# Performance work log

Hardware: AMD Instinct MI355X
Metric: run time of the kernel (lower is better)

The kernel has to match this reference:

```python
import jax, jax.numpy as jnp
import numpy as np

N = 50000        # nodes
E = 800000       # edges
D_IN = 128       # input feature dim
HID = 64         # hidden_dim
HEADS = 4
OUT = 2          # output_dim (fraud / not-fraud)
BN_EPS = 1e-5
NEG_SLOPE = 0.2  # PyG GATv2Conv default


def setup_inputs() -> dict:
    key = jax.random.key(0)
    ks = jax.random.split(key, 16)
    g = lambda k, shape, s=0.05: (jax.random.normal(k, shape, jnp.float32) * s)
    HC = HEADS * HID  # 256
    return {
        "x": jax.random.normal(ks[0], (N, D_IN), jnp.float32),
        "edge_index": jax.random.randint(ks[1], (2, E), 0, N),
        # input projection
        "W_in": g(ks[2], (D_IN, HID)), "b_in": jnp.zeros((HID,), jnp.float32),
        # GATv2 layer 0: HID -> HID, 4 heads (concat -> 256)
        "Wl0": g(ks[3], (HID, HC)), "Wr0": g(ks[4], (HID, HC)),
        "att0": g(ks[5], (HEADS, HID)), "bias0": jnp.zeros((HC,), jnp.float32),
        # GATv2 layer 1: 256 -> HID, 4 heads (concat -> 256)
        "Wl1": g(ks[6], (HC, HC)), "Wr1": g(ks[7], (HC, HC)),
        "att1": g(ks[8], (HEADS, HID)), "bias1": jnp.zeros((HC,), jnp.float32),
        # GATv2 layer 2: 256 -> OUT, 1 head
        "Wl2": g(ks[9], (HC, OUT)), "Wr2": g(ks[10], (HC, OUT)),
        "att2": g(ks[11], (1, OUT)), "bias2": jnp.zeros((OUT,), jnp.float32),
        # BatchNorm (eval mode: running stats) for the first num_layers-1 = 2 layers
        "bn_gamma": jnp.ones((2, HC), jnp.float32),
        "bn_beta": jnp.zeros((2, HC), jnp.float32),
        "bn_mean": jnp.zeros((2, HC), jnp.float32),
        "bn_var": jnp.ones((2, HC), jnp.float32),
    }


def _gatv2(h, src, dst, Wl, Wr, att, bias):
    """PyG GATv2Conv (concat=True, negative_slope=0.2). src->dst messages."""
    n = h.shape[0]
    heads, c = att.shape
    xl = (h @ Wl).reshape(n, heads, c)   # source transform
    xr = (h @ Wr).reshape(n, heads, c)   # target transform
    e = jax.nn.leaky_relu(xl[src] + xr[dst], NEG_SLOPE)       # [E, H, C]
    logits = jnp.einsum('ehc,hc->eh', e, att)                 # [E, H]
    # segment softmax over incoming edges of each destination node
    m = jax.ops.segment_max(logits, dst, num_segments=n)      # [N, H]
    ex = jnp.exp(logits - m[dst])
    denom = jax.ops.segment_sum(ex, dst, num_segments=n)
    alpha = ex / denom[dst]                                   # [E, H]
    out = jax.ops.segment_sum(xl[src] * alpha[..., None], dst, num_segments=n)
    return out.reshape(n, heads * c) + bias


def _bn_eval(h, gamma, beta, mean, var):
    return gamma * (h - mean) * jax.lax.rsqrt(var + BN_EPS) + beta


def reference(x, edge_index, W_in, b_in, Wl0, Wr0, att0, bias0,
              Wl1, Wr1, att1, bias1, Wl2, Wr2, att2, bias2,
              bn_gamma, bn_beta, bn_mean, bn_var):
    n = x.shape[0]
    loop = jnp.arange(n)
    src = jnp.concatenate([edge_index[0], loop])  # PyG add_self_loops=True
    dst = jnp.concatenate([edge_index[1], loop])

    h = jax.nn.relu(x @ W_in + b_in)              # dropout is identity in eval

    # layer 0 (no residual: 64 != 256)
    h = _gatv2(h, src, dst, Wl0, Wr0, att0, bias0)
    h = jax.nn.relu(_bn_eval(h, bn_gamma[0], bn_beta[0], bn_mean[0], bn_var[0]))

    # layer 1 (residual: 256 == 256)
    h_prev = h
    h = _gatv2(h, src, dst, Wl1, Wr1, att1, bias1)
    h = jax.nn.relu(_bn_eval(h, bn_gamma[1], bn_beta[1], bn_mean[1], bn_var[1]))
    h = h + h_prev

    # output layer, 1 head
    h = _gatv2(h, src, dst, Wl2, Wr2, att2, bias2)
    return jax.nn.log_softmax(h, axis=1)
```

## Files before the change

kernel.cpp:

```cpp
#include <hip/hip_runtime.h>
#include <hip/hip_bf16.h>
#include <math.h>


using h16     = _Float16;
using half2v  = __attribute__((ext_vector_type(2))) h16;
using half4v  = __attribute__((ext_vector_type(4))) h16;
using half8   = __attribute__((ext_vector_type(8))) h16;
using floatx2 = __attribute__((ext_vector_type(2))) float;
using floatx4 = __attribute__((ext_vector_type(4))) float;

__device__ __forceinline__ float lrelu(float x) { return x > 0.f ? x : 0.2f * x; }

__device__ __forceinline__ half2v shfl_xor_h2(half2v v, int mask) {
    float f = __builtin_bit_cast(float, v);
    f = __shfl_xor(f, mask, 64);
    return __builtin_bit_cast(half2v, f);
}

__device__ __forceinline__ half4v cvt_fp8x4(unsigned v) {
    floatx2 lo = __builtin_amdgcn_cvt_pk_f32_fp8((int)v, false);
    floatx2 hi = __builtin_amdgcn_cvt_pk_f32_fp8((int)v, true);
    half4v r = { (h16)lo.x, (h16)lo.y, (h16)hi.x, (h16)hi.y };
    return r;
}

__global__ void hist_dst(const int* __restrict__ ei, int E, int* __restrict__ deg) {
    int e = blockIdx.x * blockDim.x + threadIdx.x;
    if (e < E) atomicAdd(&deg[ei[E + e]], 1);
}

__global__ __launch_bounds__(256) void scan_blk(const int* __restrict__ deg,
                                                int* __restrict__ rowstart,
                                                int* __restrict__ bsum, int N) {
    int t = blockIdx.x * 256 + threadIdx.x;
    int lane = threadIdx.x & 63, wid = threadIdx.x >> 6;
    int v = (t < N) ? ((deg[t] + 4) & ~3) : 0;
    int x = v;
#pragma unroll
    for (int off = 1; off < 64; off <<= 1) {
        int y = __shfl_up(x, off, 64);
        if (lane >= off) x += y;
    }
    __shared__ int wsum[4];
    if (lane == 63) wsum[wid] = x;
    __syncthreads();
    int add = 0;
#pragma unroll
    for (int w = 0; w < 4; ++w) if (w < wid) add += wsum[w];
    int incl = x + add;
    if (t < N) rowstart[t] = incl - v;
    if (threadIdx.x == 255) bsum[blockIdx.x] = incl;
}

__global__ __launch_bounds__(256) void scan_off(int* __restrict__ bsum, int NB) {
    int t = threadIdx.x;
    int lane = t & 63, wid = t >> 6;
    int v = (t < NB) ? bsum[t] : 0;
    int x = v;
#pragma unroll
    for (int off = 1; off < 64; off <<= 1) {
        int y = __shfl_up(x, off, 64);
        if (lane >= off) x += y;
    }
    __shared__ int wsum[4];
    if (lane == 63) wsum[wid] = x;
    __syncthreads();
    int add = 0;
#pragma unroll
    for (int w = 0; w < 4; ++w) if (w < wid) add += wsum[w];
    if (t < NB) bsum[t] = x + add - v;
}

__global__ void add_off(const int* __restrict__ bsum, const int* __restrict__ deg,
                        int* __restrict__ rowstart, int* __restrict__ cursor,
                        int* __restrict__ csr_src, int N) {
    int t = blockIdx.x * 256 + threadIdx.x;
    if (t >= N) return;
    int r = rowstart[t] + bsum[blockIdx.x];
    rowstart[t] = r;
    cursor[t] = r;
    int dg = deg[t];
    int npad = (dg + 4) & ~3;
    for (int k = dg; k < npad; ++k) csr_src[r + k] = t;
}

__global__ void scatter_src(const int* __restrict__ ei, int E,
                            int* __restrict__ cursor, int* __restrict__ csr_src) {
    int e = blockIdx.x * blockDim.x + threadIdx.x;
    if (e >= E) return;
    int d = ei[E + e];
    int pos = atomicAdd(&cursor[d], 1);
    csr_src[pos] = ei[e];
}

__device__ __forceinline__ void pack_one(const float* __restrict__ W,
                                         h16* __restrict__ Wp,
                                         int t, int K, int NC) {
    int j = t & 7;
    int l = (t >> 3) & 63;
    int rest = t >> 9;
    int NT = NC >> 4;
    int nt = rest % NT;
    int kc = rest / NT;
    int row = kc * 32 + (l >> 4) * 8 + j;
    int col = nt * 16 + (l & 15);
    Wp[t] = (h16)W[(size_t)row * NC + col];
}

__global__ void pack_all(const float* __restrict__ W_in,
                         const float* __restrict__ Wl0, const float* __restrict__ Wr0,
                         const float* __restrict__ Wl1, const float* __restrict__ Wr1,
                         h16* __restrict__ P_in,
                         h16* __restrict__ P_l0, h16* __restrict__ P_r0,
                         h16* __restrict__ P_l1, h16* __restrict__ P_r1,
                         const float4* __restrict__ x, half4v* __restrict__ xh, int n4,
                         int* __restrict__ deg, int N) {
    int t = blockIdx.x * blockDim.x + threadIdx.x;
    if (t < 8192)        pack_one(W_in, P_in, t, 128, 64);
    else if (t < 24576)  pack_one(Wl0, P_l0, t - 8192, 64, 256);
    else if (t < 40960)  pack_one(Wr0, P_r0, t - 24576, 64, 256);
    else if (t < 106496) pack_one(Wl1, P_l1, t - 40960, 256, 256);
    else if (t < 172032) pack_one(Wr1, P_r1, t - 106496, 256, 256);
    else if (t < 172032 + n4) {
        int u = t - 172032;
        float4 v = x[u];
        half4v o = { (h16)v.x, (h16)v.y, (h16)v.z, (h16)v.w };
        xh[u] = o;
    } else {
        int u = t - 172032 - n4;
        if (u < N) deg[u] = 0;
    }
}

template<int KC, int NT, bool RELU, bool DUAL, bool OUT8>
__global__ __launch_bounds__(256) void gemm_lds(
        const h16* __restrict__ Xh,
        const h16* __restrict__ Wp0, const h16* __restrict__ Wp1,
        const float* __restrict__ bias,
        void* __restrict__ out0v, void* __restrict__ out1v, int M) {
    constexpr int K = KC * 32;
    constexpr int ldo = NT * 16;
    constexpr int CHUNK8 = NT * 64;
    constexpr int PER_THR = CHUNK8 / 256;
    __shared__ half8 wbuf[2][CHUNK8];

    const h16* Wp = (DUAL && blockIdx.y) ? Wp1 : Wp0;
    void* outv = (DUAL && blockIdx.y) ? out1v : out0v;
    const half8* WG = (const half8*)Wp;

    const int tid = threadIdx.x;
    const int wid = tid >> 6, lane = tid & 63;
    const int quad = lane >> 4, li = lane & 15;
    const int r0 = blockIdx.x * 64 + wid * 16;
    int arow = r0 + li; if (arow >= M) arow = M - 1;
    const half8* A8 = (const half8*)Xh + (size_t)arow * (K / 8) + quad;

    floatx4 acc[NT];
#pragma unroll
    for (int t = 0; t < NT; ++t) acc[t] = (floatx4){0.f, 0.f, 0.f, 0.f};

    half8 st[PER_THR];
#pragma unroll
    for (int i = 0; i < PER_THR; ++i) st[i] = WG[i * 256 + tid];
#pragma unroll
    for (int i = 0; i < PER_THR; ++i) wbuf[0][i * 256 + tid] = st[i];
    __syncthreads();

#pragma unroll
    for (int kc = 0; kc < KC; ++kc) {
        int cur = kc & 1;
        if (kc + 1 < KC) {
#pragma unroll
            for (int i = 0; i < PER_THR; ++i)
                st[i] = WG[(size_t)(kc + 1) * CHUNK8 + i * 256 + tid];
        }
        half8 a = A8[kc * 4];
#pragma unroll
        for (int nt = 0; nt < NT; ++nt) {
            half8 b = wbuf[cur][nt * 64 + lane];
            acc[nt] = __builtin_amdgcn_mfma_f32_16x16x32_f16(a, b, acc[nt], 0, 0, 0);
        }
        if (kc + 1 < KC) {
#pragma unroll
            for (int i = 0; i < PER_THR; ++i) wbuf[cur ^ 1][i * 256 + tid] = st[i];
        }
        __syncthreads();
    }

#pragma unroll
    for (int nt = 0; nt < NT; ++nt) {
#pragma unroll
        for (int reg = 0; reg < 4; ++reg) {
            int rr = r0 + quad * 4 + reg;
            if (rr >= M) continue;
            float v = acc[nt][reg];
            if (RELU) v = fmaxf(v + bias[nt * 16 + li], 0.f);
            if (OUT8) {
                int pk = __builtin_amdgcn_cvt_pk_fp8_f32(v, v, 0, false);
                ((unsigned char*)outv)[(size_t)rr * ldo + nt * 16 + li] = (unsigned char)pk;
            } else {
                ((h16*)outv)[(size_t)rr * ldo + nt * 16 + li] = (h16)v;
            }
        }
    }
}

__global__ void attn4_bn(int N, const unsigned char* __restrict__ XL8,
                         const unsigned char* __restrict__ XR8,
                         const float* __restrict__ att,
                         const int* __restrict__ rowstart, const int* __restrict__ deg,
                         const int* __restrict__ csr_src,
                         const float* __restrict__ gamma, const float* __restrict__ beta,
                         const float* __restrict__ mean, const float* __restrict__ var,
                         const float* __restrict__ bias, const float* __restrict__ resid,
                         float* __restrict__ out, h16* __restrict__ outb) {
    int d = blockIdx.x * (blockDim.x >> 6) + (threadIdx.x >> 6);
    int lane = threadIdx.x & 63;
    if (d >= N) return;
    const unsigned* XL32 = (const unsigned*)XL8;
    unsigned bw = ((const unsigned*)(XR8 + (size_t)d * 256))[lane];
    half4v bv = cvt_fp8x4(bw);
    float4 wf = ((const float4*)att)[lane];
    half2v b0 = bv.xy, b1 = bv.zw;
    half2v w0 = { (h16)wf.x, (h16)wf.y };
    half2v w1 = { (h16)wf.z, (h16)wf.w };
    const h16 k02 = (h16)0.2f;

    auto edge_part = [&](half4v xv) -> h16 {
        half2v e0 = xv.xy + b0, e1 = xv.zw + b1;
        half2v l0 = __builtin_elementwise_max(e0, e0 * k02);
        half2v l1 = __builtin_elementwise_max(e1, e1 * k02);
        half2v qd = l0 * w0 + l1 * w1;
        return qd.x + qd.y;
    };

    int start = rowstart[d];
    int nreal = deg[d] + 1;
    int npad  = (deg[d] + 4) & ~3;
    float l = 0.f;
    half2v acc0 = { (h16)0.f, (h16)0.f };
    half2v acc1 = { (h16)0.f, (h16)0.f };

    int4 iv = *(const int4*)(csr_src + start);
    for (int i = 0; i < npad; i += 8) {
        int4 ia = iv;
        int4 ib = ia;
        if (i + 4 < npad) ib = *(const int4*)(csr_src + start + i + 4);
        if (i + 8 < npad) iv = *(const int4*)(csr_src + start + i + 8);
        unsigned va0 = XL32[(size_t)ia.x * 64 + lane];
        unsigned va1 = XL32[(size_t)ia.y * 64 + lane];
        unsigned va2 = XL32[(size_t)ia.z * 64 + lane];
        unsigned va3 = XL32[(size_t)ia.w * 64 + lane];
        unsigned vb0 = XL32[(size_t)ib.x * 64 + lane];
        unsigned vb1 = XL32[(size_t)ib.y * 64 + lane];
        unsigned vb2 = XL32[(size_t)ib.z * 64 + lane];
        unsigned vb3 = XL32[(size_t)ib.w * 64 + lane];
        half4v x0 = cvt_fp8x4(va0);
        half4v x1 = cvt_fp8x4(va1);
        half4v x2 = cvt_fp8x4(va2);
        half4v x3 = cvt_fp8x4(va3);
        half4v x4 = cvt_fp8x4(vb0);
        half4v x5 = cvt_fp8x4(vb1);
        half4v x6 = cvt_fp8x4(vb2);
        half4v x7 = cvt_fp8x4(vb3);
        half2v p01 = { edge_part(x0), edge_part(x1) };
        half2v p23 = { edge_part(x2), edge_part(x3) };
        half2v p45 = { edge_part(x4), edge_part(x5) };
        half2v p67 = { edge_part(x6), edge_part(x7) };
#pragma unroll
        for (int s = 1; s < 16; s <<= 1) {
            p01 += shfl_xor_h2(p01, s);
            p23 += shfl_xor_h2(p23, s);
            p45 += shfl_xor_h2(p45, s);
            p67 += shfl_xor_h2(p67, s);
        }
        int rem = nreal - i;
        float e0 = __expf((float)p01.x);
        float e1 = (rem > 1) ? __expf((float)p01.y) : 0.f;
        float e2 = (rem > 2) ? __expf((float)p23.x) : 0.f;
        float e3 = (rem > 3) ? __expf((float)p23.y) : 0.f;
        float e4 = (rem > 4) ? __expf((float)p45.x) : 0.f;
        float e5 = (rem > 5) ? __expf((float)p45.y) : 0.f;
        float e6 = (rem > 6) ? __expf((float)p67.x) : 0.f;
        float e7 = (rem > 7) ? __expf((float)p67.y) : 0.f;
        l += ((e0 + e1) + (e2 + e3)) + ((e4 + e5) + (e6 + e7));
        h16 h0 = (h16)e0, h1 = (h16)e1, h2 = (h16)e2, h3 = (h16)e3;
        h16 h4 = (h16)e4, h5 = (h16)e5, h6 = (h16)e6, h7 = (h16)e7;
        half2v eb0 = { h0, h0 }, eb1 = { h1, h1 }, eb2 = { h2, h2 }, eb3 = { h3, h3 };
        half2v eb4 = { h4, h4 }, eb5 = { h5, h5 }, eb6 = { h6, h6 }, eb7 = { h7, h7 };
        acc0 += eb0 * x0.xy; acc1 += eb0 * x0.zw;
        acc0 += eb1 * x1.xy; acc1 += eb1 * x1.zw;
        acc0 += eb2 * x2.xy; acc1 += eb2 * x2.zw;
        acc0 += eb3 * x3.xy; acc1 += eb3 * x3.zw;
        acc0 += eb4 * x4.xy; acc1 += eb4 * x4.zw;
        acc0 += eb5 * x5.xy; acc1 += eb5 * x5.zw;
        acc0 += eb6 * x6.xy; acc1 += eb6 * x6.zw;
        acc0 += eb7 * x7.xy; acc1 += eb7 * x7.zw;
    }
    float4 acc = { (float)acc0.x, (float)acc0.y, (float)acc1.x, (float)acc1.y };
    float inv = 1.f / l;
    float4 g  = ((const float4*)gamma)[lane];
    float4 be = ((const float4*)beta)[lane];
    float4 mu = ((const float4*)mean)[lane];
    float4 va = ((const float4*)var)[lane];
    float4 bi = ((const float4*)bias)[lane];
    float4 sc4, sh4;
    sc4.x = g.x * rsqrtf(va.x + 1e-5f); sh4.x = (bi.x - mu.x) * sc4.x + be.x;
    sc4.y = g.y * rsqrtf(va.y + 1e-5f); sh4.y = (bi.y - mu.y) * sc4.y + be.y;
    sc4.z = g.z * rsqrtf(va.z + 1e-5f); sh4.z = (bi.z - mu.z) * sc4.z + be.z;
    sc4.w = g.w * rsqrtf(va.w + 1e-5f); sh4.w = (bi.w - mu.w) * sc4.w + be.w;
    float4 o;
    o.x = fmaxf(acc.x * inv * sc4.x + sh4.x, 0.f);
    o.y = fmaxf(acc.y * inv * sc4.y + sh4.y, 0.f);
    o.z = fmaxf(acc.z * inv * sc4.z + sh4.z, 0.f);
    o.w = fmaxf(acc.w * inv * sc4.w + sh4.w, 0.f);
    if (resid) {
        float4 rv = *(const float4*)(resid + (size_t)d * 256 + lane * 4);
        o.x += rv.x; o.y += rv.y; o.z += rv.z; o.w += rv.w;
    }
    if (out) *(float4*)(out + (size_t)d * 256 + lane * 4) = o;
    if (outb) {
        half4v ob = { (h16)o.x, (h16)o.y, (h16)o.z, (h16)o.w };
        *(half4v*)(outb + (size_t)d * 256 + lane * 4) = ob;
    }
}

__global__ void gemm2_wave(const h16* __restrict__ X, const float* __restrict__ Wl,
                           const float* __restrict__ Wr, float* __restrict__ xl2,
                           float* __restrict__ xr2, int N) {
    int t = blockIdx.x * blockDim.x + threadIdx.x;
    int n = t >> 4;
    int sl = t & 15;
    if (n >= N) return;
    const half4v* Xr = (const half4v*)(X + (size_t)n * 256);
    const float4* Wl4 = (const float4*)Wl;
    const float4* Wr4 = (const float4*)Wr;
    float l0 = 0.f, l1 = 0.f, r0 = 0.f, r1 = 0.f;
#pragma unroll
    for (int j = 0; j < 4; ++j) {
        int idx = sl + j * 16;
        half4v xh = Xr[idx];
        float4 xv = { (float)xh.x, (float)xh.y, (float)xh.z, (float)xh.w };
        float4 wa = Wl4[idx * 2];
        float4 wb = Wl4[idx * 2 + 1];
        l0 += xv.x * wa.x + xv.y * wa.z + xv.z * wb.x + xv.w * wb.z;
        l1 += xv.x * wa.y + xv.y * wa.w + xv.z * wb.y + xv.w * wb.w;
        wa = Wr4[idx * 2]; wb = Wr4[idx * 2 + 1];
        r0 += xv.x * wa.x + xv.y * wa.z + xv.z * wb.x + xv.w * wb.z;
        r1 += xv.x * wa.y + xv.y * wa.w + xv.z * wb.y + xv.w * wb.w;
    }
#pragma unroll
    for (int off = 1; off < 16; off <<= 1) {
        l0 += __shfl_xor(l0, off, 64);
        l1 += __shfl_xor(l1, off, 64);
        r0 += __shfl_xor(r0, off, 64);
        r1 += __shfl_xor(r1, off, 64);
    }
    if (sl == 0) {
        xl2[n * 2] = l0; xl2[n * 2 + 1] = l1;
        xr2[n * 2] = r0; xr2[n * 2 + 1] = r1;
    }
}

__global__ void attn1_16(int N, const float* __restrict__ xl2, const float* __restrict__ xr2,
                         const float* __restrict__ att, const float* __restrict__ bias,
                         const int* __restrict__ rowstart, const int* __restrict__ deg,
                         const int* __restrict__ csr_src, float* __restrict__ out) {
    int t = blockIdx.x * blockDim.x + threadIdx.x;
    int d = t >> 4, sl = t & 15;
    if (d >= N) return;
    float a0 = att[0], a1 = att[1];
    float2 xr = ((const float2*)xr2)[d];
    float b0 = xr.x, b1 = xr.y;
    int st = rowstart[d];
    int nreal = deg[d] + 1;
    int npad  = (deg[d] + 4) & ~3;
    float l = 0.f, ac0 = 0.f, ac1 = 0.f;
    for (int i = sl; i < npad; i += 16) {
        int s = csr_src[st + i];
        float2 xv = ((const float2*)xl2)[s];
        float q = lrelu(xv.x + b0) * a0 + lrelu(xv.y + b1) * a1;
        float e = (i < nreal) ? __expf(q) : 0.f;
        l += e; ac0 += e * xv.x; ac1 += e * xv.y;
    }
#pragma unroll
    for (int off = 1; off < 16; off <<= 1) {
        l   += __shfl_xor(l, off, 64);
        ac0 += __shfl_xor(ac0, off, 64);
        ac1 += __shfl_xor(ac1, off, 64);
    }
    if (sl == 0) {
        float inv = 1.f / l;
        float v0 = ac0 * inv + bias[0];
        float v1 = ac1 * inv + bias[1];
        float mx = fmaxf(v0, v1);
        float lse = mx + logf(__expf(v0 - mx) + __expf(v1 - mx));
        out[d * 2] = v0 - lse;
        out[d * 2 + 1] = v1 - lse;
    }
}

extern "C" void kernel_launch(void* const* d_in, const int* in_sizes, int n_in,
                              void* d_out, int out_size, void* d_ws, size_t ws_size,
                              hipStream_t stream) {
    const float* x        = (const float*)d_in[0];
    const int*   ei       = (const int*)  d_in[1];
    const float* W_in     = (const float*)d_in[2];
    const float* b_in     = (const float*)d_in[3];
    const float* Wl0      = (const float*)d_in[4];
    const float* Wr0      = (const float*)d_in[5];
    const float* att0     = (const float*)d_in[6];
    const float* bias0    = (const float*)d_in[7];
    const float* Wl1      = (const float*)d_in[8];
    const float* Wr1      = (const float*)d_in[9];
    const float* att1     = (const float*)d_in[10];
    const float* bias1    = (const float*)d_in[11];
    const float* Wl2      = (const float*)d_in[12];
    const float* Wr2      = (const float*)d_in[13];
    const float* att2     = (const float*)d_in[14];
    const float* bias2    = (const float*)d_in[15];
    const float* bn_gamma = (const float*)d_in[16];
    const float* bn_beta  = (const float*)d_in[17];
    const float* bn_mean  = (const float*)d_in[18];
    const float* bn_var   = (const float*)d_in[19];

    const int N  = in_sizes[0] / 128;
    const int E  = in_sizes[1] / 2;
    const int NB = (N + 255) / 256;

    float* ws = (float*)d_ws;
    size_t off = 0;
    float* C    = ws + off; off += (size_t)N * 256;
    float* XL2  = ws + off; off += (size_t)N * 2;
    float* XR2  = ws + off; off += (size_t)N * 2;
    unsigned char* A8 = (unsigned char*)(ws + off); off += (size_t)N * 64;
    unsigned char* B8 = (unsigned char*)(ws + off); off += (size_t)N * 64;
    h16* Ch   = (h16*)(ws + off); off += (size_t)N * 128;
    h16* Dh   = (h16*)(ws + off); off += (size_t)N * 128;
    h16* H0h  = (h16*)(ws + off); off += (size_t)N * 32;
    h16* xh   = (h16*)(ws + off); off += (size_t)N * 64;
    h16* Wp_in = (h16*)(ws + off); off += 4096;
    h16* Wp_l0 = (h16*)(ws + off); off += 8192;
    h16* Wp_r0 = (h16*)(ws + off); off += 8192;
    h16* Wp_l1 = (h16*)(ws + off); off += 32768;
    h16* Wp_r1 = (h16*)(ws + off); off += 32768;
    int* ip = (int*)(ws + off);
    int* deg      = ip;              ip += N;
    int* rowstart = ip;              ip += N;
    int* cursor   = ip;              ip += N;
    int* bsum     = ip;              ip += NB;
    int* csr_src  = ip;              ip += E + 4 * N + 64;

    const int PACK_T = 172032 + N * 32 + N;
    pack_all<<<(PACK_T + 255) / 256, 256, 0, stream>>>(
        W_in, Wl0, Wr0, Wl1, Wr1, Wp_in, Wp_l0, Wp_r0, Wp_l1, Wp_r1,
        (const float4*)x, (half4v*)xh, N * 32, deg, N);

    hist_dst<<<(E + 255) / 256, 256, 0, stream>>>(ei, E, deg);
    scan_blk<<<NB, 256, 0, stream>>>(deg, rowstart, bsum, N);
    scan_off<<<1, 256, 0, stream>>>(bsum, NB);
    add_off<<<NB, 256, 0, stream>>>(bsum, deg, rowstart, cursor, csr_src, N);
    scatter_src<<<(E + 255) / 256, 256, 0, stream>>>(ei, E, cursor, csr_src);

    const int GBM = (N + 63) / 64;

    gemm_lds<4, 4, true, false, false><<<GBM, 256, 0, stream>>>(
        xh, Wp_in, nullptr, b_in, H0h, nullptr, N);

    gemm_lds<2, 16, false, true, true><<<dim3(GBM, 2), 256, 0, stream>>>(
        H0h, Wp_l0, Wp_r0, nullptr, A8, B8, N);
    attn4_bn<<<(N + 3) / 4, 256, 0, stream>>>(N, A8, B8, att0, rowstart, deg, csr_src,
                                              bn_gamma, bn_beta, bn_mean, bn_var,
                                              bias0, nullptr, C, Ch);

    gemm_lds<8, 16, false, true, true><<<dim3(GBM, 2), 256, 0, stream>>>(
        Ch, Wp_l1, Wp_r1, nullptr, A8, B8, N);
    attn4_bn<<<(N + 3) / 4, 256, 0, stream>>>(N, A8, B8, att1, rowstart, deg, csr_src,
                                              bn_gamma + 256, bn_beta + 256, bn_mean + 256,
                                              bn_var + 256, bias1, C, nullptr, Dh);

    gemm2_wave<<<(N * 16 + 255) / 256, 256, 0, stream>>>(Dh, Wl2, Wr2, XL2, XR2, N);
    attn1_16<<<(N * 16 + 255) / 256, 256, 0, stream>>>(N, XL2, XR2, att2, bias2,
                                                       rowstart, deg, csr_src, (float*)d_out);
}
```

Measured before the change: 424.2 us.

## Store GAT projections in fp16 instead of fp8 and drop fp32 residual buffer

The dual projection GEMMs now write fp16 XL/XR instead of fp8, so the attention kernel loads 8 bytes per lane and skips the fp8-to-half conversion. The residual path now reads the fp16 layer-0 output instead of a separate fp32 copy, which removes that fp32 write and read. The gather loop processes 4 edges per iteration instead of 8. This doubles the gather traffic for neighbour features and lowers memory-level parallelism per iteration, in exchange for better accuracy and fewer conversion instructions.

```diff
diff --git a/kernel.cpp b/kernel.cpp
--- a/kernel.cpp
+++ b/kernel.cpp
@@ -16,13 +16,6 @@
     float f = __builtin_bit_cast(float, v);
     f = __shfl_xor(f, mask, 64);
     return __builtin_bit_cast(half2v, f);
-}
-
-__device__ __forceinline__ half4v cvt_fp8x4(unsigned v) {
-    floatx2 lo = __builtin_amdgcn_cvt_pk_f32_fp8((int)v, false);
-    floatx2 hi = __builtin_amdgcn_cvt_pk_f32_fp8((int)v, true);
-    half4v r = { (h16)lo.x, (h16)lo.y, (h16)hi.x, (h16)hi.y };
-    return r;
 }
 
 __global__ void hist_dst(const int* __restrict__ ei, int E, int* __restrict__ deg) {
@@ -133,12 +126,12 @@
     }
 }
 
-template<int KC, int NT, bool RELU, bool DUAL, bool OUT8>
+template<int KC, int NT, bool RELU, bool DUAL>
 __global__ __launch_bounds__(256) void gemm_lds(
         const h16* __restrict__ Xh,
         const h16* __restrict__ Wp0, const h16* __restrict__ Wp1,
         const float* __restrict__ bias,
-        void* __restrict__ out0v, void* __restrict__ out1v, int M) {
+        h16* __restrict__ out0, h16* __restrict__ out1, int M) {
     constexpr int K = KC * 32;
     constexpr int ldo = NT * 16;
     constexpr int CHUNK8 = NT * 64;
@@ -146,7 +139,7 @@
     __shared__ half8 wbuf[2][CHUNK8];
 
     const h16* Wp = (DUAL && blockIdx.y) ? Wp1 : Wp0;
-    void* outv = (DUAL && blockIdx.y) ? out1v : out0v;
+    h16* outp = (DUAL && blockIdx.y) ? out1 : out0;
     const half8* WG = (const half8*)Wp;
 
     const int tid = threadIdx.x;
@@ -196,31 +189,25 @@
             if (rr >= M) continue;
             float v = acc[nt][reg];
             if (RELU) v = fmaxf(v + bias[nt * 16 + li], 0.f);
-            if (OUT8) {
-                int pk = __builtin_amdgcn_cvt_pk_fp8_f32(v, v, 0, false);
-                ((unsigned char*)outv)[(size_t)rr * ldo + nt * 16 + li] = (unsigned char)pk;
-            } else {
-                ((h16*)outv)[(size_t)rr * ldo + nt * 16 + li] = (h16)v;
-            }
+            outp[(size_t)rr * ldo + nt * 16 + li] = (h16)v;
         }
     }
 }
 
-__global__ void attn4_bn(int N, const unsigned char* __restrict__ XL8,
-                         const unsigned char* __restrict__ XR8,
+__global__ void attn4_bn(int N, const h16* __restrict__ XL,
+                         const h16* __restrict__ XR,
                          const float* __restrict__ att,
                          const int* __restrict__ rowstart, const int* __restrict__ deg,
                          const int* __restrict__ csr_src,
                          const float* __restrict__ gamma, const float* __restrict__ beta,
                          const float* __restrict__ mean, const float* __restrict__ var,
-                         const float* __restrict__ bias, const float* __restrict__ resid,
-                         float* __restrict__ out, h16* __restrict__ outb) {
+                         const float* __restrict__ bias, const h16* __restrict__ resid,
+                         h16* __restrict__ outb) {
     int d = blockIdx.x * (blockDim.x >> 6) + (threadIdx.x >> 6);
     int lane = threadIdx.x & 63;
     if (d >= N) return;
-    const unsigned* XL32 = (const unsigned*)XL8;
-    unsigned bw = ((const unsigned*)(XR8 + (size_t)d * 256))[lane];
-    half4v bv = cvt_fp8x4(bw);
+    const uint2* XL64 = (const uint2*)XL;
+    half4v bv = *(const half4v*)(XR + (size_t)d * 256 + lane * 4);
     float4 wf = ((const float4*)att)[lane];
     half2v b0 = bv.xy, b1 = bv.zw;
     half2v w0 = { (h16)wf.x, (h16)wf.y };
@@ -243,60 +230,36 @@
     half2v acc1 = { (h16)0.f, (h16)0.f };
 
     int4 iv = *(const int4*)(csr_src + start);
-    for (int i = 0; i < npad; i += 8) {
-        int4 ia = iv;
-        int4 ib = ia;
-        if (i + 4 < npad) ib = *(const int4*)(csr_src + start + i + 4);
-        if (i + 8 < npad) iv = *(const int4*)(csr_src + start + i + 8);
-        unsigned va0 = XL32[(size_t)ia.x * 64 + lane];
-        unsigned va1 = XL32[(size_t)ia.y * 64 + lane];
-        unsigned va2 = XL32[(size_t)ia.z * 64 + lane];
-        unsigned va3 = XL32[(size_t)ia.w * 64 + lane];
-        unsigned vb0 = XL32[(size_t)ib.x * 64 + lane];
-        unsigned vb1 = XL32[(size_t)ib.y * 64 + lane];
-        unsigned vb2 = XL32[(size_t)ib.z * 64 + lane];
-        unsigned vb3 = XL32[(size_t)ib.w * 64 + lane];
-        half4v x0 = cvt_fp8x4(va0);
-        half4v x1 = cvt_fp8x4(va1);
-        half4v x2 = cvt_fp8x4(va2);
-        half4v x3 = cvt_fp8x4(va3);
-        half4v x4 = cvt_fp8x4(vb0);
-        half4v x5 = cvt_fp8x4(vb1);
-        half4v x6 = cvt_fp8x4(vb2);
-        half4v x7 = cvt_fp8x4(vb3);
+    for (int i = 0; i < npad; i += 4) {
+        int4 cur = iv;
+        if (i + 4 < npad) iv = *(const int4*)(csr_src + start + i + 4);
+        uint2 v0 = XL64[(size_t)cur.x * 64 + lane];
+        uint2 v1 = XL64[(size_t)cur.y * 64 + lane];
+        uint2 v2 = XL64[(size_t)cur.z * 64 + lane];
+        uint2 v3 = XL64[(size_t)cur.w * 64 + lane];
+        half4v x0 = __builtin_bit_cast(half4v, v0);
+        half4v x1 = __builtin_bit_cast(half4v, v1);
+        half4v x2 = __builtin_bit_cast(half4v, v2);
+        half4v x3 = __builtin_bit_cast(half4v, v3);
         half2v p01 = { edge_part(x0), edge_part(x1) };
         half2v p23 = { edge_part(x2), edge_part(x3) };
-        half2v p45 = { edge_part(x4), edge_part(x5) };
-        half2v p67 = { edge_part(x6), edge_part(x7) };
 #pragma unroll
         for (int s = 1; s < 16; s <<= 1) {
             p01 += shfl_xor_h2(p01, s);
             p23 += shfl_xor_h2(p23, s);
-            p45 += shfl_xor_h2(p45, s);
-            p67 += shfl_xor_h2(p67, s);
         }
         int rem = nreal - i;
         float e0 = __expf((float)p01.x);
         float e1 = (rem > 1) ? __expf((float)p01.y) : 0.f;
         float e2 = (rem > 2) ? __expf((float)p23.x) : 0.f;
         float e3 = (rem > 3) ? __expf((float)p23.y) : 0.f;
-        float e4 = (rem > 4) ? __expf((float)p45.x) : 0.f;
-        float e5 = (rem > 5) ? __expf((float)p45.y) : 0.f;
-        float e6 = (rem > 6) ? __expf((float)p67.x) : 0.f;
-        float e7 = (rem > 7) ? __expf((float)p67.y) : 0.f;
-        l += ((e0 + e1) + (e2 + e3)) + ((e4 + e5) + (e6 + e7));
+        l += (e0 + e1) + (e2 + e3);
         h16 h0 = (h16)e0, h1 = (h16)e1, h2 = (h16)e2, h3 = (h16)e3;
-        h16 h4 = (h16)e4, h5 = (h16)e5, h6 = (h16)e6, h7 = (h16)e7;
         half2v eb0 = { h0, h0 }, eb1 = { h1, h1 }, eb2 = { h2, h2 }, eb3 = { h3, h3 };
-        half2v eb4 = { h4, h4 }, eb5 = { h5, h5 }, eb6 = { h6, h6 }, eb7 = { h7, h7 };
         acc0 += eb0 * x0.xy; acc1 += eb0 * x0.zw;
         acc0 += eb1 * x1.xy; acc1 += eb1 * x1.zw;
         acc0 += eb2 * x2.xy; acc1 += eb2 * x2.zw;
         acc0 += eb3 * x3.xy; acc1 += eb3 * x3.zw;
-        acc0 += eb4 * x4.xy; acc1 += eb4 * x4.zw;
-        acc0 += eb5 * x5.xy; acc1 += eb5 * x5.zw;
-        acc0 += eb6 * x6.xy; acc1 += eb6 * x6.zw;
-        acc0 += eb7 * x7.xy; acc1 += eb7 * x7.zw;
     }
     float4 acc = { (float)acc0.x, (float)acc0.y, (float)acc1.x, (float)acc1.y };
     float inv = 1.f / l;
@@ -316,14 +279,12 @@
     o.z = fmaxf(acc.z * inv * sc4.z + sh4.z, 0.f);
     o.w = fmaxf(acc.w * inv * sc4.w + sh4.w, 0.f);
     if (resid) {
-        float4 rv = *(const float4*)(resid + (size_t)d * 256 + lane * 4);
-        o.x += rv.x; o.y += rv.y; o.z += rv.z; o.w += rv.w;
-    }
-    if (out) *(float4*)(out + (size_t)d * 256 + lane * 4) = o;
-    if (outb) {
-        half4v ob = { (h16)o.x, (h16)o.y, (h16)o.z, (h16)o.w };
-        *(half4v*)(outb + (size_t)d * 256 + lane * 4) = ob;
-    }
+        half4v rv = *(const half4v*)(resid + (size_t)d * 256 + lane * 4);
+        o.x += (float)rv.x; o.y += (float)rv.y;
+        o.z += (float)rv.z; o.w += (float)rv.w;
+    }
+    half4v ob = { (h16)o.x, (h16)o.y, (h16)o.z, (h16)o.w };
+    *(half4v*)(outb + (size_t)d * 256 + lane * 4) = ob;
 }
 
 __global__ void gemm2_wave(const h16* __restrict__ X, const float* __restrict__ Wl,
@@ -431,11 +392,10 @@
 
     float* ws = (float*)d_ws;
     size_t off = 0;
-    float* C    = ws + off; off += (size_t)N * 256;
     float* XL2  = ws + off; off += (size_t)N * 2;
     float* XR2  = ws + off; off += (size_t)N * 2;
-    unsigned char* A8 = (unsigned char*)(ws + off); off += (size_t)N * 64;
-    unsigned char* B8 = (unsigned char*)(ws + off); off += (size_t)N * 64;
+    h16* Ah   = (h16*)(ws + off); off += (size_t)N * 128;
+    h16* Bh   = (h16*)(ws + off); off += (size_t)N * 128;
     h16* Ch   = (h16*)(ws + off); off += (size_t)N * 128;
     h16* Dh   = (h16*)(ws + off); off += (size_t)N * 128;
     h16* H0h  = (h16*)(ws + off); off += (size_t)N * 32;
@@ -465,20 +425,20 @@
 
     const int GBM = (N + 63) / 64;
 
-    gemm_lds<4, 4, true, false, false><<<GBM, 256, 0, stream>>>(
+    gemm_lds<4, 4, true, false><<<GBM, 256, 0, stream>>>(
         xh, Wp_in, nullptr, b_in, H0h, nullptr, N);
 
-    gemm_lds<2, 16, false, true, true><<<dim3(GBM, 2), 256, 0, stream>>>(
-        H0h, Wp_l0, Wp_r0, nullptr, A8, B8, N);
-    attn4_bn<<<(N + 3) / 4, 256, 0, stream>>>(N, A8, B8, att0, rowstart, deg, csr_src,
+    gemm_lds<2, 16, false, true><<<dim3(GBM, 2), 256, 0, stream>>>(
+        H0h, Wp_l0, Wp_r0, nullptr, Ah, Bh, N);
+    attn4_bn<<<(N + 3) / 4, 256, 0, stream>>>(N, Ah, Bh, att0, rowstart, deg, csr_src,
                                               bn_gamma, bn_beta, bn_mean, bn_var,
-                                              bias0, nullptr, C, Ch);
-
-    gemm_lds<8, 16, false, true, true><<<dim3(GBM, 2), 256, 0, stream>>>(
-        Ch, Wp_l1, Wp_r1, nullptr, A8, B8, N);
-    attn4_bn<<<(N + 3) / 4, 256, 0, stream>>>(N, A8, B8, att1, rowstart, deg, csr_src,
+                                              bias0, nullptr, Ch);
+
+    gemm_lds<8, 16, false, true><<<dim3(GBM, 2), 256, 0, stream>>>(
+        Ch, Wp_l1, Wp_r1, nullptr, Ah, Bh, N);
+    attn4_bn<<<(N + 3) / 4, 256, 0, stream>>>(N, Ah, Bh, att1, rowstart, deg, csr_src,
                                               bn_gamma + 256, bn_beta + 256, bn_mean + 256,
-                                              bn_var + 256, bias1, C, nullptr, Dh);
+                                              bn_var + 256, bias1, Ch, Dh);
 
     gemm2_wave<<<(N * 16 + 255) / 256, 256, 0, stream>>>(Dh, Wl2, Wr2, XL2, XR2, N);
     attn1_16<<<(N * 16 + 255) / 256, 256, 0, stream>>>(N, XL2, XR2, att2, bias2,
```

New measurement: 415.9 us. -2.0%, faster.
